# Performance work log

Measured on AMD Instinct MI355X. Metric: run time of the kernel, lower is better.

Reference implementation:

```python
import jax, jax.numpy as jnp
import numpy as np

IMAGE_SIZE = 256


def setup_inputs():
    B, A, S, C = 2, 3, 8, 20
    key = jax.random.key(0)
    k1, k2, k3, k4, k5, k6 = jax.random.split(key, 6)
    predictions = jax.random.normal(k1, (B, A, S, S, 6 + C), dtype=jnp.float32)
    obj = (jax.random.uniform(k2, (B, A, S, S)) < 0.15).astype(jnp.float32)
    txy = jax.random.uniform(k3, (B, A, S, S, 2), minval=0.05, maxval=0.95)
    twh = jax.random.uniform(k4, (B, A, S, S, 2), minval=0.3, maxval=3.0)
    cls = jax.random.randint(k5, (B, A, S, S), 0, C).astype(jnp.float32)
    target = jnp.concatenate([obj[..., None], txy, twh, cls[..., None]], axis=-1)
    anchors = jnp.array([[0.9, 1.6], [2.2, 3.0], [4.8, 6.1]], dtype=jnp.float32)
    depth_target = jax.random.uniform(k6, (B, IMAGE_SIZE, IMAGE_SIZE), minval=0.0, maxval=80.0)
    return {"predictions": predictions, "target": target, "anchors": anchors,
            "depth_target": depth_target, "S": S}


def _bce_logits_masked(x, y, m):
    # BCEWithLogitsLoss (mean) restricted to mask m
    l = jnp.maximum(x, 0.0) - x * y + jnp.log1p(jnp.exp(-jnp.abs(x)))
    mf = m.astype(x.dtype)
    return (l * mf).sum() / jnp.maximum(mf.sum(), 1.0)


def _iou_midpoint(a, b):
    ax1, ax2 = a[..., 0] - a[..., 2] / 2, a[..., 0] + a[..., 2] / 2
    ay1, ay2 = a[..., 1] - a[..., 3] / 2, a[..., 1] + a[..., 3] / 2
    bx1, bx2 = b[..., 0] - b[..., 2] / 2, b[..., 0] + b[..., 2] / 2
    by1, by2 = b[..., 1] - b[..., 3] / 2, b[..., 1] + b[..., 3] / 2
    iw = jnp.clip(jnp.minimum(ax2, bx2) - jnp.maximum(ax1, bx1), 0.0)
    ih = jnp.clip(jnp.minimum(ay2, by2) - jnp.maximum(ay1, by1), 0.0)
    inter = iw * ih
    area_a = jnp.abs((ax2 - ax1) * (ay2 - ay1))
    area_b = jnp.abs((bx2 - bx1) * (by2 - by1))
    return inter / (area_a + area_b - inter + 1e-6)


def _silog_masked(pred, tgt, m):
    # SILogLoss with boolean mask; torch.var is unbiased (n-1)
    mf = m.astype(jnp.float32)
    n = mf.sum()
    g = (jnp.log(jnp.maximum(pred, 1e-30)) - jnp.log(jnp.maximum(tgt, 1e-30))) * mf
    mean = g.sum() / jnp.maximum(n, 1.0)
    var = (((g - mean) ** 2) * mf).sum() / jnp.maximum(n - 1.0, 1.0)
    Dg = var + 0.15 * mean ** 2
    return 10.0 * jnp.sqrt(jnp.maximum(Dg, 1e-30)), n


def _axis_mask(lo, hi, L):
    # replicate python slice semantics a[int(lo):int(hi)] (trunc toward 0, negative wrap)
    lo = jnp.trunc(jnp.clip(lo, -1e9, 1e9)).astype(jnp.int32)
    hi = jnp.trunc(jnp.clip(hi, -1e9, 1e9)).astype(jnp.int32)
    lo = jnp.where(lo < 0, jnp.maximum(L + lo, 0), jnp.minimum(lo, L))
    hi = jnp.where(hi < 0, jnp.maximum(L + hi, 0), jnp.minimum(hi, L))
    r = jnp.arange(L)
    return (r >= lo) & (r < hi)


def reference(predictions, target, anchors, depth_target, S):
    B, A = predictions.shape[0], predictions.shape[1]
    IMG = depth_target.shape[-1]
    objf = (target[..., 0] == 1.0).astype(jnp.float32)
    noobj = target[..., 0] == 0.0
    n_obj = jnp.maximum(objf.sum(), 1.0)

    no_object_loss = _bce_logits_masked(predictions[..., 0], target[..., 0], noobj)

    anch = anchors.reshape(1, A, 1, 1, 2)
    box_preds = jnp.concatenate([jax.nn.sigmoid(predictions[..., 1:3]),
                                 jnp.exp(predictions[..., 3:5]) * anch], axis=-1)
    ious = jax.lax.stop_gradient(_iou_midpoint(box_preds, target[..., 1:5]))
    object_loss = (((jax.nn.sigmoid(predictions[..., 0]) - ious * target[..., 0]) ** 2) * objf).sum() / n_obj

    # in-place mutation in original: predictions[...,1:3] = sigmoid(...)
    pred_xy = jax.nn.sigmoid(predictions[..., 1:3])
    tgt_box = jnp.concatenate([target[..., 1:3], jnp.log(1e-16 + target[..., 3:5] / anch)], axis=-1)
    pred_box = jnp.concatenate([pred_xy, predictions[..., 3:5]], axis=-1)
    box_loss = (((pred_box - tgt_box) ** 2) * objf[..., None]).sum() / (n_obj * 4.0)

    logp = jax.nn.log_softmax(predictions[..., 6:], axis=-1)
    labels = target[..., 5].astype(jnp.int32)
    nll = -jnp.take_along_axis(logp, labels[..., None], axis=-1)[..., 0]
    class_loss = (nll * objf).sum() / n_obj

    # depth rasterization loop; cells_to_bboxes mutates predictions in place, so
    # each outer k iteration compounds sigmoid on xy and exp*anchor on wh
    xy, wh = pred_xy, predictions[..., 3:5]
    cxs, cys, ws, hs, vs = [], [], [], [], []
    jj = jnp.arange(S)[None, None, None, :].astype(jnp.float32)
    ii = jnp.arange(S)[None, None, :, None].astype(jnp.float32)
    for k in range(A):
        xy = jax.nn.sigmoid(xy)
        wh = jnp.exp(wh) * anch
        cx = (xy[..., 0] + jj) / S * IMG
        cy = (xy[..., 1] + ii) / S * IMG
        w = wh[..., 0] / S * IMG
        h = wh[..., 1] / S * IMG
        # loop order in source: k, i, j, b -> layout [S, S, B] per k
        cxs.append(jnp.transpose(cx[:, k], (1, 2, 0)))
        cys.append(jnp.transpose(cy[:, k], (1, 2, 0)))
        ws.append(jnp.transpose(w[:, k], (1, 2, 0)))
        hs.append(jnp.transpose(h[:, k], (1, 2, 0)))
        vs.append(jnp.transpose(predictions[:, k, :, :, 5], (1, 2, 0)))
    floats = jnp.stack([jnp.stack(cxs).ravel(), jnp.stack(cys).ravel(),
                        jnp.stack(ws).ravel(), jnp.stack(hs).ravel(),
                        jnp.stack(vs).ravel()], axis=-1)  # [T,5]
    bidx = jnp.broadcast_to(jnp.arange(B), (A, S, S, B)).reshape(-1)

    @jax.checkpoint
    def step(carry, inp):
        dp, ds, loss, cnt = carry
        f, b = inp
        cx, cy, w, h, v = f[0], f[1], f[2], f[3], f[4]
        valid = (w > 0) & (h > 0) & jnp.isfinite(w) & jnp.isfinite(h)
        val = jnp.maximum(1.0, v)
        bm = (jnp.arange(B) == b)[:, None, None]
        rf = _axis_mask(cx - w / 2, cx + w / 2, IMG)[:, None] & _axis_mask(cy - h / 2, cy + h / 2, IMG)[None, :]
        rs = _axis_mask(cx - w / 4, cx + w / 4, IMG)[:, None] & _axis_mask(cy - h / 4, cy + h / 4, IMG)[None, :]
        dp = jnp.where(valid & bm & rf[None], val, dp)
        ds = jnp.where(valid & bm & rs[None], val, ds)
        mf = (depth_target >= 1.0) & (dp >= 1.0)
        pl1, n1 = _silog_masked(dp, depth_target, mf)
        add1 = valid & (n1 >= 2.0)  # n==1 -> unbiased var NaN -> skipped in torch
        loss = loss + jnp.where(add1, pl1, 0.0)
        cnt = cnt + add1.astype(jnp.float32)
        ms = (depth_target >= 1.0) & (ds >= 1.0)
        pl2, n2 = _silog_masked(ds, depth_target, ms)
        add2 = valid & (n2 >= 2.0)
        loss = loss + jnp.where(add2, pl2, 0.0)
        cnt = cnt + add2.astype(jnp.float32)
        return (dp, ds, loss, cnt), None

    init = (jnp.zeros_like(depth_target), jnp.zeros_like(depth_target),
            jnp.float32(0.0), jnp.float32(0.0))
    (_, _, dloss, cnt), _ = jax.lax.scan(step, init, (floats, bidx))
    depth_loss = dloss / jnp.maximum(cnt, 1.0)

    return (10.0 * box_loss + 1.0 * object_loss + 10.0 * no_object_loss
            + 1.0 * class_loss + 1.0 * depth_loss)
```

## Files before the change

### kernel.cpp

```cpp
#include <hip/hip_runtime.h>
#include <cmath>

#define BN 2
#define AN 3
#define SN 8
#define CN 20
#define IMGN 256
#define NSTEP 384
#define PRED_C 26
#define NE (NSTEP * 6)
#define NBB 256
#define NSB (NSTEP / BN)
#define NRB 36

__device__ __forceinline__ float wredf(float v){
  #pragma unroll
  for (int o = 32; o; o >>= 1) v += __shfl_xor(v, o);
  return v;
}
__device__ __forceinline__ double wredd(double v){
  #pragma unroll
  for (int o = 32; o; o >>= 1) v += __shfl_xor(v, o);
  return v;
}
__device__ __forceinline__ float wsum_dpp(float x){
  x += __int_as_float(__builtin_amdgcn_update_dpp(0, __float_as_int(x), 0x111, 0xf, 0xf, false));
  x += __int_as_float(__builtin_amdgcn_update_dpp(0, __float_as_int(x), 0x112, 0xf, 0xf, false));
  x += __int_as_float(__builtin_amdgcn_update_dpp(0, __float_as_int(x), 0x114, 0xf, 0xf, false));
  x += __int_as_float(__builtin_amdgcn_update_dpp(0, __float_as_int(x), 0x118, 0xf, 0xf, false));
  x += __int_as_float(__builtin_amdgcn_update_dpp(0, __float_as_int(x), 0x142, 0xa, 0xf, false));
  x += __int_as_float(__builtin_amdgcn_update_dpp(0, __float_as_int(x), 0x143, 0xc, 0xf, false));
  return x;
}
__device__ __forceinline__ int finitef(float x){
  return (__float_as_uint(x) & 0x7f800000u) != 0x7f800000u;
}
__device__ __forceinline__ unsigned axism(float lo, float hi){
  float lof = truncf(fminf(fmaxf(lo, -1e9f), 1e9f));
  float hif = truncf(fminf(fmaxf(hi, -1e9f), 1e9f));
  int l = (int)lof, h = (int)hif;
  l = (l < 0) ? max(IMGN + l, 0) : min(l, IMGN);
  h = (h < 0) ? max(IMGN + h, 0) : min(h, IMGN);
  return (unsigned)l | ((unsigned)h << 16);
}

__device__ __forceinline__ void step_params(int t, const float* __restrict__ pred,
                                            const float* __restrict__ anc,
                                            unsigned* valid, float* lv,
                                            unsigned* fx, unsigned* fy,
                                            unsigned* sx, unsigned* sy){
  int b = t % BN;
  int j = (t / BN) % SN;
  int i = (t / (BN * SN)) % SN;
  int k = t / (BN * SN * SN);
  const float* pc = pred + (size_t)((((b * AN + k) * SN + i) * SN + j)) * PRED_C;
  float x = pc[1], y = pc[2], wv = pc[3], hv = pc[4], v = pc[5];
  float aw = anc[2 * k], ah = anc[2 * k + 1];
  for (int m = 0; m < k + 2; ++m) {
    x = 1.0f / (1.0f + expf(-x));
    y = 1.0f / (1.0f + expf(-y));
  }
  for (int m = 0; m < k + 1; ++m) {
    wv = expf(wv) * aw;
    hv = expf(hv) * ah;
  }
  float cx = (x + (float)j) / 8.0f * 256.0f;
  float cy = (y + (float)i) / 8.0f * 256.0f;
  float w  = wv / 8.0f * 256.0f;
  float h  = hv / 8.0f * 256.0f;
  *valid = (w > 0.0f) && (h > 0.0f) && finitef(w) && finitef(h);
  *lv = logf(fmaxf(1.0f, v));
  *fx = axism(cx - w / 2.0f, cx + w / 2.0f);
  *fy = axism(cy - h / 2.0f, cy + h / 2.0f);
  *sx = axism(cx - w / 4.0f, cx + w / 4.0f);
  *sy = axism(cy - h / 4.0f, cy + h / 4.0f);
}

__global__ __launch_bounds__(512) void yolo_kB(const float* __restrict__ pred,
                                               const float* __restrict__ anc,
                                               const float* __restrict__ depth,
                                               float* __restrict__ scratch){
  __shared__ uint2    s_rxx[NSTEP];
  __shared__ uint2    s_cyy[NSTEP];
  __shared__ float    s_lv[NSTEP];
  __shared__ uint4    s_clist[8][NSB];
  __shared__ int      s_nact[8];
  __shared__ float    s_acc[NE];

  int tid = threadIdx.x;
  for (int t = tid; t < NSTEP; t += 512) {
    unsigned vld, fx, fy, sx, sy; float lv;
    step_params(t, pred, anc, &vld, &lv, &fx, &fy, &sx, &sy);
    if (!vld) { fx = 0xFFFFu; sx = 0xFFFFu; }
    s_rxx[t] = make_uint2(fx, sx);
    s_cyy[t] = make_uint2(fy, sy);
    s_lv[t] = lv;
  }
  for (int e = tid; e < NE; e += 512) s_acc[e] = 0.0f;
  __syncthreads();

  int half = tid >> 8;
  int ru = blockIdx.x * 2 + half;
  int b = ru >> 8, r = ru & 255;
  int c = tid & 255, ln = tid & 63, w = tid >> 6;
  int wlo = c & ~63, whi = wlo + 64;

  {
    int cnt = 0;
    #pragma unroll
    for (int g = 0; g < 3; ++g) {
      int m = g * 64 + ln;
      int t = b + 2 * m;
      uint2 rx = s_rxx[t];
      uint2 cy = s_cyy[t];
      bool rowF = (r >= (int)(rx.x & 0xffffu)) && (r < (int)(rx.x >> 16));
      bool rowS = (r >= (int)(rx.y & 0xffffu)) && (r < (int)(rx.y >> 16));
      bool fF = rowF && ((int)(cy.x & 0xffffu) < whi) && ((int)(cy.x >> 16) > wlo);
      bool fS = rowS && ((int)(cy.y & 0xffffu) < whi) && ((int)(cy.y >> 16) > wlo);
      bool f = fF || fS;
      unsigned long long msk = __ballot(f);
      int pos = (int)__popcll(msk & ((1ull << ln) - 1ull));
      if (f) {
        unsigned tf = (unsigned)t | (fF ? 512u : 0u) | (fS ? 1024u : 0u);
        s_clist[w][cnt + pos] = make_uint4(cy.x, cy.y, __float_as_uint(s_lv[t]), tf);
      }
      cnt += (int)__popcll(msk);
    }
    if (ln == 0) s_nact[w] = cnt;
  }

  float dt = depth[(size_t)ru * IMGN + c];
  bool okp = dt >= 1.0f;
  float ldt = okp ? logf(dt) : 0.0f;
  int ce = okp ? c : 0x7fffffff;
  __syncthreads();
  int nact = s_nact[w];

  unsigned long long hFmask = 0ull, hSmask = 0ull;
  float lvF = ldt, lvS = ldt;
  float ldt2 = 2.0f * ldt;
  int idx = 0;
  while (idx < nact) {
    uint4 E0 = s_clist[w][idx];
    bool two = (idx + 1 < nact);
    uint4 E1 = two ? s_clist[w][idx + 1] : make_uint4(0u, 0u, 0u, 0u);
    idx += 2;
    float lv0 = __uint_as_float(E0.z), lv1 = __uint_as_float(E1.z);
    bool inF0 = (E0.w & 512u)  && (ce >= (int)(E0.x & 0xffffu)) && (ce < (int)(E0.x >> 16));
    bool inS0 = (E0.w & 1024u) && (ce >= (int)(E0.y & 0xffffu)) && (ce < (int)(E0.y >> 16));
    bool inF1 = (E1.w & 512u)  && (ce >= (int)(E1.x & 0xffffu)) && (ce < (int)(E1.x >> 16));
    bool inS1 = (E1.w & 1024u) && (ce >= (int)(E1.y & 0xffffu)) && (ce < (int)(E1.y >> 16));
    unsigned long long aF0 = __ballot(inF0), aS0 = __ballot(inS0);
    unsigned long long aF1 = __ballot(inF1), aS1 = __ballot(inS1);
    if ((aF0 | aS0 | aF1 | aS1) == 0ull) continue;
    unsigned long long mF0 = aF0 & ~hFmask; hFmask |= aF0;
    unsigned long long mF1 = aF1 & ~hFmask; hFmask |= aF1;
    unsigned long long mS0 = aS0 & ~hSmask; hSmask |= aS0;
    unsigned long long mS1 = aS1 & ~hSmask; hSmask |= aS1;
    float d10 = inF0 ? (lv0 - lvF) : 0.0f;
    float d20 = d10 * (lv0 + lvF - ldt2);
    lvF = inF0 ? lv0 : lvF;
    float d11 = inF1 ? (lv1 - lvF) : 0.0f;
    float d21 = d11 * (lv1 + lvF - ldt2);
    lvF = inF1 ? lv1 : lvF;
    float g10 = inS0 ? (lv0 - lvS) : 0.0f;
    float g20 = g10 * (lv0 + lvS - ldt2);
    lvS = inS0 ? lv0 : lvS;
    float g11 = inS1 ? (lv1 - lvS) : 0.0f;
    float g21 = g11 * (lv1 + lvS - ldt2);
    lvS = inS1 ? lv1 : lvS;
    if (aF0 | aF1) { d10 = wsum_dpp(d10); d20 = wsum_dpp(d20);
                     d11 = wsum_dpp(d11); d21 = wsum_dpp(d21); }
    if (aS0 | aS1) { g10 = wsum_dpp(g10); g20 = wsum_dpp(g20);
                     g11 = wsum_dpp(g11); g21 = wsum_dpp(g21); }
    if (ln == 63) {
      float* b0 = s_acc + (int)(E0.w & 511u) * 6;
      float c00 = (float)__popcll(mF0), c30 = (float)__popcll(mS0);
      if (c00 != 0.f) atomicAdd(b0 + 0, c00);
      if (d10 != 0.f) atomicAdd(b0 + 1, d10);
      if (d20 != 0.f) atomicAdd(b0 + 2, d20);
      if (c30 != 0.f) atomicAdd(b0 + 3, c30);
      if (g10 != 0.f) atomicAdd(b0 + 4, g10);
      if (g20 != 0.f) atomicAdd(b0 + 5, g20);
      if (two) {
        float* b1 = s_acc + (int)(E1.w & 511u) * 6;
        float c01 = (float)__popcll(mF1), c31 = (float)__popcll(mS1);
        if (c01 != 0.f) atomicAdd(b1 + 0, c01);
        if (d11 != 0.f) atomicAdd(b1 + 1, d11);
        if (d21 != 0.f) atomicAdd(b1 + 2, d21);
        if (c31 != 0.f) atomicAdd(b1 + 3, c31);
        if (g11 != 0.f) atomicAdd(b1 + 4, g11);
        if (g21 != 0.f) atomicAdd(b1 + 5, g21);
      }
    }
  }
  __syncthreads();
  for (int e = tid; e < NE; e += 512)
    scratch[(size_t)blockIdx.x * NE + e] = s_acc[e];
}

__global__ __launch_bounds__(256) void yolo_kR(const float* __restrict__ scratch,
                                               double* __restrict__ reduced){
  __shared__ double part[4][64];
  int ln = threadIdx.x & 63, w = threadIdx.x >> 6;
  int e = blockIdx.x * 64 + ln;
  const float* p = scratch + e;
  double s0 = 0, s1 = 0, s2 = 0, s3 = 0, s4 = 0, s5 = 0, s6 = 0, s7 = 0;
  int bk0 = w * (NBB / 4);
  for (int bk = bk0; bk < bk0 + NBB / 4; bk += 8) {
    s0 += (double)p[(size_t)(bk + 0) * NE];
    s1 += (double)p[(size_t)(bk + 1) * NE];
    s2 += (double)p[(size_t)(bk + 2) * NE];
    s3 += (double)p[(size_t)(bk + 3) * NE];
    s4 += (double)p[(size_t)(bk + 4) * NE];
    s5 += (double)p[(size_t)(bk + 5) * NE];
    s6 += (double)p[(size_t)(bk + 6) * NE];
    s7 += (double)p[(size_t)(bk + 7) * NE];
  }
  part[w][ln] = ((s0 + s1) + (s2 + s3)) + ((s4 + s5) + (s6 + s7));
  __syncthreads();
  if (w == 0)
    reduced[e] = part[0][ln] + part[1][ln] + part[2][ln] + part[3][ln];
}

__global__ __launch_bounds__(384) void yolo_kC(const float* __restrict__ pred,
                                               const float* __restrict__ tgt,
                                               const float* __restrict__ anc,
                                               const double* __restrict__ reduced,
                                               float* __restrict__ out){
  __shared__ double sd[NE];
  __shared__ double chunk[6 * 6];
  __shared__ double rl[6], rc[6];
  __shared__ float  ry[6 * 6];
  int tid = threadIdx.x;
  for (int e = tid; e < NE; e += 384) sd[e] = reduced[e];

  float s_obj, s_bce, s_bcecnt, s_objls, s_boxls, s_clsls;
  {
    int t = tid;
    int j = t % SN;
    int i = (t / SN) % SN;
    int a = (t / (SN * SN)) % AN;
    int b = t / (SN * SN * AN);
    const float* pc = pred + (size_t)((((b * AN + a) * SN + i) * SN + j)) * PRED_C;
    const float* tc = tgt  + (size_t)((((b * AN + a) * SN + i) * SN + j)) * 6;
    float t0 = tc[0];
    float objf  = (t0 == 1.0f) ? 1.0f : 0.0f;
    float noobj = (t0 == 0.0f) ? 1.0f : 0.0f;
    float p0 = pc[0];
    float l = fmaxf(p0, 0.0f) - p0 * t0 + log1pf(expf(-fabsf(p0)));
    s_bce = l * noobj; s_bcecnt = noobj; s_obj = objf;
    float aw = anc[2 * a], ah = anc[2 * a + 1];
    float sxp = 1.0f / (1.0f + expf(-pc[1]));
    float syp = 1.0f / (1.0f + expf(-pc[2]));
    float bw = expf(pc[3]) * aw, bh = expf(pc[4]) * ah;
    float ax1 = sxp - bw * 0.5f, ax2 = sxp + bw * 0.5f;
    float ay1 = syp - bh * 0.5f, ay2 = syp + bh * 0.5f;
    float bx1 = tc[1] - tc[3] * 0.5f, bx2 = tc[1] + tc[3] * 0.5f;
    float by1 = tc[2] - tc[4] * 0.5f, by2 = tc[2] + tc[4] * 0.5f;
    float iw = fmaxf(fminf(ax2, bx2) - fmaxf(ax1, bx1), 0.0f);
    float ih = fmaxf(fminf(ay2, by2) - fmaxf(ay1, by1), 0.0f);
    float inter = iw * ih;
    float areaA = fabsf((ax2 - ax1) * (ay2 - ay1));
    float areaB = fabsf((bx2 - bx1) * (by2 - by1));
    float iou = inter / (areaA + areaB - inter + 1e-6f);
    float sp0 = 1.0f / (1.0f + expf(-p0));
    float od = sp0 - iou * t0;
    s_objls = od * od * objf;
    float dx = sxp - tc[1], dy = syp - tc[2];
    float dw = pc[3] - logf(1e-16f + tc[3] / aw);
    float dh = pc[4] - logf(1e-16f + tc[4] / ah);
    s_boxls = (dx * dx + dy * dy + dw * dw + dh * dh) * objf;
    int lbl = (int)tc[5];
    float mx = -INFINITY;
    for (int c = 0; c < CN; ++c) mx = fmaxf(mx, pc[6 + c]);
    float se = 0.0f;
    for (int c = 0; c < CN; ++c) se += expf(pc[6 + c] - mx);
    float nll = mx + logf(se) - pc[6 + lbl];
    s_clsls = nll * objf;
  }
  {
    int wv = tid >> 6, ln = tid & 63;
    float vals[6] = { s_obj, s_bce, s_bcecnt, s_objls, s_boxls, s_clsls };
    #pragma unroll
    for (int ci = 0; ci < 6; ++ci) {
      float v = wredf(vals[ci]);
      if (ln == 0) ry[ci * 6 + wv] = v;
    }
  }

  unsigned vld, ufx, ufy, usx, usy; float ulv;
  step_params(tid, pred, anc, &vld, &ulv, &ufx, &ufy, &usx, &usy);

  __syncthreads();
  {
    int ch = tid >> 6, ln = tid & 63;
    #pragma unroll
    for (int comp = 0; comp < 6; ++comp) {
      double v = wredd(sd[(ch * 64 + ln) * 6 + comp]);
      if (ln == 0) chunk[ch * 6 + comp] = v;
    }
  }
  __syncthreads();

  int t = tid;
  int ch = t >> 6;
  double P[6];
  #pragma unroll
  for (int comp = 0; comp < 6; ++comp) {
    double s = 0.0;
    for (int cc = 0; cc < ch; ++cc) s += chunk[cc * 6 + comp];
    for (int tt = (ch << 6); tt <= t; ++tt) s += sd[tt * 6 + comp];
    P[comp] = s;
  }
  double lossd = 0.0, cntd = 0.0;
  {
    double n = P[0], Sg = P[1], Sg2 = P[2];
    double mean = Sg / fmax(n, 1.0);
    double var = (Sg2 - 2.0 * mean * Sg + n * mean * mean) / fmax(n - 1.0, 1.0);
    double Dg = var + 0.15 * mean * mean;
    double pl = 10.0 * sqrt(fmax(Dg, 1e-30));
    if (vld && n >= 2.0) { lossd += pl; cntd += 1.0; }
  }
  {
    double n = P[3], Sg = P[4], Sg2 = P[5];
    double mean = Sg / fmax(n, 1.0);
    double var = (Sg2 - 2.0 * mean * Sg + n * mean * mean) / fmax(n - 1.0, 1.0);
    double Dg = var + 0.15 * mean * mean;
    double pl = 10.0 * sqrt(fmax(Dg, 1e-30));
    if (vld && n >= 2.0) { lossd += pl; cntd += 1.0; }
  }
  int wv = tid >> 6, ln = tid & 63;
  double L = wredd(lossd), C = wredd(cntd);
  if (ln == 0) { rl[wv] = L; rc[wv] = C; }
  __syncthreads();
  if (tid == 0) {
    double totL = 0.0, totC = 0.0;
    for (int i = 0; i < 6; ++i) { totL += rl[i]; totC += rc[i]; }
    float yolo[6];
    #pragma unroll
    for (int ci = 0; ci < 6; ++ci) {
      float s = 0.0f;
      for (int w2 = 0; w2 < 6; ++w2) s += ry[ci * 6 + w2];
      yolo[ci] = s;
    }
    float dl = (float)(totL / fmax(totC, 1.0));
    float nobj = fmaxf(yolo[0], 1.0f);
    float noo  = yolo[1] / fmaxf(yolo[2], 1.0f);
    float objl = yolo[3] / nobj;
    float boxl = yolo[4] / (nobj * 4.0f);
    float clsl = yolo[5] / nobj;
    out[0] = 10.0f * boxl + objl + 10.0f * noo + clsl + dl;
  }
}

extern "C" void kernel_launch(void* const* d_in, const int* in_sizes, int n_in,
                              void* d_out, int out_size, void* d_ws, size_t ws_size,
                              hipStream_t stream) {
  const float* pred  = (const float*)d_in[0];
  const float* tgt   = (const float*)d_in[1];
  const float* anc   = (const float*)d_in[2];
  const float* depth = (const float*)d_in[3];

  float*  scratch = (float*)d_ws;
  double* reduced = (double*)((char*)d_ws + (size_t)NBB * NE * sizeof(float));

  hipLaunchKernelGGL(yolo_kB, dim3(NBB), dim3(512), 0, stream, pred, anc, depth, scratch);
  hipLaunchKernelGGL(yolo_kR, dim3(NRB), dim3(256), 0, stream, scratch, reduced);
  hipLaunchKernelGGL(yolo_kC, dim3(1), dim3(384), 0, stream, pred, tgt, anc, reduced, (float*)d_out);
}
```

Baseline: 119.8 us.

## Split full and shrunk box masks across separate waves, one image row per block

Each block now handles a single image row instead of two. Its eight waves are split so four handle the full-box mask and four handle the shrunk-box mask for 64-column windows, which removes the dual-mask bookkeeping, the extra ballots and the extra DPP reductions per candidate. The block count doubles to 512, so the scratch buffer and the reduction kernel now read twice as many partials. Per-step setup in shared memory is also repeated across twice as many blocks.

```diff
diff --git a/kernel.cpp b/kernel.cpp
--- a/kernel.cpp
+++ b/kernel.cpp
@@ -9,7 +9,7 @@
 #define NSTEP 384
 #define PRED_C 26
 #define NE (NSTEP * 6)
-#define NBB 256
+#define NB (BN * IMGN)
 #define NSB (NSTEP / BN)
 #define NRB 36
 
@@ -99,11 +99,12 @@
   for (int e = tid; e < NE; e += 512) s_acc[e] = 0.0f;
   __syncthreads();
 
-  int half = tid >> 8;
-  int ru = blockIdx.x * 2 + half;
+  int ru = blockIdx.x;
   int b = ru >> 8, r = ru & 255;
-  int c = tid & 255, ln = tid & 63, w = tid >> 6;
-  int wlo = c & ~63, whi = wlo + 64;
+  int ln = tid & 63, w = tid >> 6;
+  int win = w & 3, type = w >> 2;
+  int wlo = win * 64, whi = wlo + 64;
+  int c = wlo + ln;
 
   {
     int cnt = 0;
@@ -113,17 +114,13 @@
       int t = b + 2 * m;
       uint2 rx = s_rxx[t];
       uint2 cy = s_cyy[t];
-      bool rowF = (r >= (int)(rx.x & 0xffffu)) && (r < (int)(rx.x >> 16));
-      bool rowS = (r >= (int)(rx.y & 0xffffu)) && (r < (int)(rx.y >> 16));
-      bool fF = rowF && ((int)(cy.x & 0xffffu) < whi) && ((int)(cy.x >> 16) > wlo);
-      bool fS = rowS && ((int)(cy.y & 0xffffu) < whi) && ((int)(cy.y >> 16) > wlo);
-      bool f = fF || fS;
+      unsigned rb = type ? rx.y : rx.x;
+      unsigned cb = type ? cy.y : cy.x;
+      bool rowT = (r >= (int)(rb & 0xffffu)) && (r < (int)(rb >> 16));
+      bool f = rowT && ((int)(cb & 0xffffu) < whi) && ((int)(cb >> 16) > wlo);
       unsigned long long msk = __ballot(f);
       int pos = (int)__popcll(msk & ((1ull << ln) - 1ull));
-      if (f) {
-        unsigned tf = (unsigned)t | (fF ? 512u : 0u) | (fS ? 1024u : 0u);
-        s_clist[w][cnt + pos] = make_uint4(cy.x, cy.y, __float_as_uint(s_lv[t]), tf);
-      }
+      if (f) s_clist[w][cnt + pos] = make_uint4(cb, __float_as_uint(s_lv[t]), (unsigned)t, 0u);
       cnt += (int)__popcll(msk);
     }
     if (ln == 0) s_nact[w] = cnt;
@@ -136,61 +133,43 @@
   __syncthreads();
   int nact = s_nact[w];
 
-  unsigned long long hFmask = 0ull, hSmask = 0ull;
-  float lvF = ldt, lvS = ldt;
+  unsigned long long hmask = 0ull;
+  float lvP = ldt;
   float ldt2 = 2.0f * ldt;
+  int coff = type * 3;
   int idx = 0;
   while (idx < nact) {
     uint4 E0 = s_clist[w][idx];
     bool two = (idx + 1 < nact);
-    uint4 E1 = two ? s_clist[w][idx + 1] : make_uint4(0u, 0u, 0u, 0u);
+    uint4 E1 = two ? s_clist[w][idx + 1] : make_uint4(0xFFFFu, 0u, 0u, 0u);
     idx += 2;
-    float lv0 = __uint_as_float(E0.z), lv1 = __uint_as_float(E1.z);
-    bool inF0 = (E0.w & 512u)  && (ce >= (int)(E0.x & 0xffffu)) && (ce < (int)(E0.x >> 16));
-    bool inS0 = (E0.w & 1024u) && (ce >= (int)(E0.y & 0xffffu)) && (ce < (int)(E0.y >> 16));
-    bool inF1 = (E1.w & 512u)  && (ce >= (int)(E1.x & 0xffffu)) && (ce < (int)(E1.x >> 16));
-    bool inS1 = (E1.w & 1024u) && (ce >= (int)(E1.y & 0xffffu)) && (ce < (int)(E1.y >> 16));
-    unsigned long long aF0 = __ballot(inF0), aS0 = __ballot(inS0);
-    unsigned long long aF1 = __ballot(inF1), aS1 = __ballot(inS1);
-    if ((aF0 | aS0 | aF1 | aS1) == 0ull) continue;
-    unsigned long long mF0 = aF0 & ~hFmask; hFmask |= aF0;
-    unsigned long long mF1 = aF1 & ~hFmask; hFmask |= aF1;
-    unsigned long long mS0 = aS0 & ~hSmask; hSmask |= aS0;
-    unsigned long long mS1 = aS1 & ~hSmask; hSmask |= aS1;
-    float d10 = inF0 ? (lv0 - lvF) : 0.0f;
-    float d20 = d10 * (lv0 + lvF - ldt2);
-    lvF = inF0 ? lv0 : lvF;
-    float d11 = inF1 ? (lv1 - lvF) : 0.0f;
-    float d21 = d11 * (lv1 + lvF - ldt2);
-    lvF = inF1 ? lv1 : lvF;
-    float g10 = inS0 ? (lv0 - lvS) : 0.0f;
-    float g20 = g10 * (lv0 + lvS - ldt2);
-    lvS = inS0 ? lv0 : lvS;
-    float g11 = inS1 ? (lv1 - lvS) : 0.0f;
-    float g21 = g11 * (lv1 + lvS - ldt2);
-    lvS = inS1 ? lv1 : lvS;
-    if (aF0 | aF1) { d10 = wsum_dpp(d10); d20 = wsum_dpp(d20);
-                     d11 = wsum_dpp(d11); d21 = wsum_dpp(d21); }
-    if (aS0 | aS1) { g10 = wsum_dpp(g10); g20 = wsum_dpp(g20);
-                     g11 = wsum_dpp(g11); g21 = wsum_dpp(g21); }
+    float lv0 = __uint_as_float(E0.y), lv1 = __uint_as_float(E1.y);
+    bool in0 = (ce >= (int)(E0.x & 0xffffu)) && (ce < (int)(E0.x >> 16));
+    bool in1 = (ce >= (int)(E1.x & 0xffffu)) && (ce < (int)(E1.x >> 16));
+    unsigned long long a0 = __ballot(in0), a1 = __ballot(in1);
+    if ((a0 | a1) == 0ull) continue;
+    unsigned long long m0 = a0 & ~hmask; hmask |= a0;
+    unsigned long long m1 = a1 & ~hmask; hmask |= a1;
+    float d10 = in0 ? (lv0 - lvP) : 0.0f;
+    float d20 = d10 * (lv0 + lvP - ldt2);
+    lvP = in0 ? lv0 : lvP;
+    float d11 = in1 ? (lv1 - lvP) : 0.0f;
+    float d21 = d11 * (lv1 + lvP - ldt2);
+    lvP = in1 ? lv1 : lvP;
+    d10 = wsum_dpp(d10); d20 = wsum_dpp(d20);
+    d11 = wsum_dpp(d11); d21 = wsum_dpp(d21);
     if (ln == 63) {
-      float* b0 = s_acc + (int)(E0.w & 511u) * 6;
-      float c00 = (float)__popcll(mF0), c30 = (float)__popcll(mS0);
-      if (c00 != 0.f) atomicAdd(b0 + 0, c00);
+      float* b0 = s_acc + (int)E0.z * 6 + coff;
+      float c0 = (float)__popcll(m0);
+      if (c0  != 0.f) atomicAdd(b0 + 0, c0);
       if (d10 != 0.f) atomicAdd(b0 + 1, d10);
       if (d20 != 0.f) atomicAdd(b0 + 2, d20);
-      if (c30 != 0.f) atomicAdd(b0 + 3, c30);
-      if (g10 != 0.f) atomicAdd(b0 + 4, g10);
-      if (g20 != 0.f) atomicAdd(b0 + 5, g20);
       if (two) {
-        float* b1 = s_acc + (int)(E1.w & 511u) * 6;
-        float c01 = (float)__popcll(mF1), c31 = (float)__popcll(mS1);
-        if (c01 != 0.f) atomicAdd(b1 + 0, c01);
+        float* b1 = s_acc + (int)E1.z * 6 + coff;
+        float c1 = (float)__popcll(m1);
+        if (c1  != 0.f) atomicAdd(b1 + 0, c1);
         if (d11 != 0.f) atomicAdd(b1 + 1, d11);
         if (d21 != 0.f) atomicAdd(b1 + 2, d21);
-        if (c31 != 0.f) atomicAdd(b1 + 3, c31);
-        if (g11 != 0.f) atomicAdd(b1 + 4, g11);
-        if (g21 != 0.f) atomicAdd(b1 + 5, g21);
       }
     }
   }
@@ -206,8 +185,8 @@
   int e = blockIdx.x * 64 + ln;
   const float* p = scratch + e;
   double s0 = 0, s1 = 0, s2 = 0, s3 = 0, s4 = 0, s5 = 0, s6 = 0, s7 = 0;
-  int bk0 = w * (NBB / 4);
-  for (int bk = bk0; bk < bk0 + NBB / 4; bk += 8) {
+  int bk0 = w * (NB / 4);
+  for (int bk = bk0; bk < bk0 + NB / 4; bk += 8) {
     s0 += (double)p[(size_t)(bk + 0) * NE];
     s1 += (double)p[(size_t)(bk + 1) * NE];
     s2 += (double)p[(size_t)(bk + 2) * NE];
@@ -363,9 +342,9 @@
   const float* depth = (const float*)d_in[3];
 
   float*  scratch = (float*)d_ws;
-  double* reduced = (double*)((char*)d_ws + (size_t)NBB * NE * sizeof(float));
-
-  hipLaunchKernelGGL(yolo_kB, dim3(NBB), dim3(512), 0, stream, pred, anc, depth, scratch);
+  double* reduced = (double*)((char*)d_ws + (size_t)NB * NE * sizeof(float));
+
+  hipLaunchKernelGGL(yolo_kB, dim3(NB), dim3(512), 0, stream, pred, anc, depth, scratch);
   hipLaunchKernelGGL(yolo_kR, dim3(NRB), dim3(256), 0, stream, scratch, reduced);
   hipLaunchKernelGGL(yolo_kC, dim3(1), dim3(384), 0, stream, pred, tgt, anc, reduced, (float*)d_out);
 }
```

After: 112.2 us. 1.07x faster.
